# Performance work log

Measured on AMD Instinct MI355X. Metric: run time of the kernel, lower is better.

The kernel has to match this reference:

```python
import jax, jax.numpy as jnp
import numpy as np

N, E, D = 50000, 800000, 128
EPS = 1e-5  # PyG BatchNorm default eps


def setup_inputs() -> dict:
    key = jax.random.key(0)
    ks = jax.random.split(key, 12)
    s = 1.0 / np.sqrt(D)
    x = jax.random.normal(ks[0], (N, D), jnp.float32)
    edge_index = jax.random.randint(ks[1], (2, E), 0, N, dtype=jnp.int32)
    Wp = jax.random.normal(ks[2], (D, D), jnp.float32) * s
    bp = jax.random.normal(ks[3], (D,), jnp.float32) * 0.01
    # 4 SAGEConv layers, all 128->128, stacked: lin_l (neighbor, with bias) and lin_r (root)
    Wl = jax.random.normal(ks[4], (4, D, D), jnp.float32) * s
    bl = jax.random.normal(ks[5], (4, D), jnp.float32) * 0.01
    Wr = jax.random.normal(ks[6], (4, D, D), jnp.float32) * s
    # BatchNorm params/buffers (eval mode: running stats)
    bn_gamma = 1.0 + 0.1 * jax.random.normal(ks[7], (4, D), jnp.float32)
    bn_beta = 0.1 * jax.random.normal(ks[8], (4, D), jnp.float32)
    bn_mean = 0.1 * jax.random.normal(ks[9], (4, D), jnp.float32)
    bn_var = jax.random.uniform(ks[10], (4, D), jnp.float32, 0.5, 1.5)
    return {"x": x, "edge_index": edge_index, "Wp": Wp, "bp": bp, "Wl": Wl,
            "bl": bl, "Wr": Wr, "bn_gamma": bn_gamma, "bn_beta": bn_beta,
            "bn_mean": bn_mean, "bn_var": bn_var}


def _sage_conv(x, src, dst, inv_deg, Wl, bl, Wr):
    # mean-aggregate neighbor features: gather x[src], scatter-sum to dst, divide by degree
    agg = jax.ops.segment_sum(x[src], dst, num_segments=N) * inv_deg  # [N, D]
    # PyG SAGEConv: lin_l(aggr) + lin_r(x_root)
    return agg @ Wl + bl + x @ Wr


def _bn(h, gamma, beta, mean, var):
    return (h - mean) * (gamma * jax.lax.rsqrt(var + EPS)) + beta


def reference(x, edge_index, Wp, bp, Wl, bl, Wr, bn_gamma, bn_beta, bn_mean, bn_var):
    src, dst = edge_index[0], edge_index[1]
    deg = jax.ops.segment_sum(jnp.ones((E,), x.dtype), dst, num_segments=N)
    inv_deg = (1.0 / jnp.maximum(deg, 1.0))[:, None]  # [N, 1]
    x = jax.nn.relu(x @ Wp + bp)
    # eval mode: dropout is identity, BN uses running stats
    for i in range(3):
        h = _sage_conv(x, src, dst, inv_deg, Wl[i], bl[i], Wr[i])
        h = jax.nn.relu(_bn(h, bn_gamma[i], bn_beta[i], bn_mean[i], bn_var[i]))
        x = x + h
    x = _sage_conv(x, src, dst, inv_deg, Wl[3], bl[3], Wr[3])
    return jax.nn.relu(_bn(x, bn_gamma[3], bn_beta[3], bn_mean[3], bn_var[3]))
```

## Files before the change

kernel.cpp:

```cpp
#include <hip/hip_runtime.h>

#define DIM 128
#define BN_EPS 1e-5f
#define BCAP 8192
#define EPB 4096
#define EPT 16

typedef __bf16 bf16x8 __attribute__((ext_vector_type(8)));
typedef float f32x4 __attribute__((ext_vector_type(4)));
typedef float f32x2 __attribute__((ext_vector_type(2)));

__device__ __forceinline__ float bf_e0(unsigned int u) {
    return __builtin_bit_cast(float, u << 16);
}
__device__ __forceinline__ float bf_e1(unsigned int u) {
    return __builtin_bit_cast(float, u & 0xffff0000u);
}
__device__ __forceinline__ unsigned short f2b(float f) {
    __bf16 b = (__bf16)f;
    return __builtin_bit_cast(unsigned short, b);
}
__device__ __forceinline__ unsigned int pack2(float lo, float hi) {
    return (unsigned int)f2b(lo) | ((unsigned int)f2b(hi) << 16);
}

__global__ __launch_bounds__(256) void k_bin(const int* __restrict__ src,
                                             const int* __restrict__ dst,
                                             int* __restrict__ cursor,
                                             unsigned int* __restrict__ binned,
                                             int E, int NB) {
    __shared__ int hist[256];
    __shared__ int base[256];
    __shared__ int c2[256];
    const int tid = threadIdx.x;
    const int e0 = blockIdx.x * EPB;

    unsigned int u[EPT];
    int b[EPT];
    hist[tid] = 0;
    c2[tid] = 0;
    __syncthreads();
#pragma unroll
    for (int i = 0; i < EPT; ++i) {
        int e = e0 + i * 256 + tid;
        if (e < E) {
            int d = dst[e];
            b[i] = d >> 8;
            u[i] = ((unsigned int)(d & 255) << 17) | (unsigned int)src[e];
            atomicAdd(&hist[b[i]], 1);
        } else {
            b[i] = -1;
        }
    }
    __syncthreads();
    if (tid < NB && hist[tid] > 0) base[tid] = atomicAdd(&cursor[tid], hist[tid]);
    __syncthreads();
#pragma unroll
    for (int i = 0; i < EPT; ++i) {
        if (b[i] < 0) continue;
        int p = base[b[i]] + atomicAdd(&c2[b[i]], 1);
        if (p < BCAP) binned[(size_t)b[i] * BCAP + p] = u[i];
    }
}

__global__ __launch_bounds__(256) void k_bscan(const int* __restrict__ cursor,
                                               int* __restrict__ bbase,
                                               int* __restrict__ rowptr, int NB,
                                               int N, int E) {
    __shared__ int sh[256];
    int t = threadIdx.x;
    int v = (t < NB) ? min(cursor[t], BCAP) : 0;
    sh[t] = v;
    __syncthreads();
    for (int off = 1; off < 256; off <<= 1) {
        int a = (t >= off) ? sh[t - off] : 0;
        __syncthreads();
        sh[t] += a;
        __syncthreads();
    }
    if (t < NB) bbase[t] = sh[t] - v;
    if (t == 0) rowptr[N] = E;
}

__global__ __launch_bounds__(256) void k_csr(const int* __restrict__ cursor,
                                             const int* __restrict__ bbase,
                                             const unsigned int* __restrict__ binned,
                                             int* __restrict__ rowptr,
                                             float* __restrict__ inv_deg,
                                             int* __restrict__ col, int N) {
    __shared__ unsigned int stage[BCAP];
    __shared__ int deg[256];
    __shared__ int start[256];
    const int b = blockIdx.x;
    const int t = threadIdx.x;
    const int node0 = b << 8;
    const int cnt = min(cursor[b], BCAP);
    const int gbase = bbase[b];

    deg[t] = 0;
    __syncthreads();
    for (int e = t; e < cnt; e += 256) {
        unsigned int u = binned[(size_t)b * BCAP + e];
        stage[e] = u;
        atomicAdd(&deg[u >> 17], 1);
    }
    __syncthreads();
    int d = deg[t];
    start[t] = d;
    __syncthreads();
    for (int off = 1; off < 256; off <<= 1) {
        int a = (t >= off) ? start[t - off] : 0;
        __syncthreads();
        start[t] += a;
        __syncthreads();
    }
    int excl = start[t] - d;
    int node = node0 + t;
    if (node < N) {
        rowptr[node] = gbase + excl;
        inv_deg[node] = 1.0f / (float)(d > 1 ? d : 1);
    }
    __syncthreads();
    deg[t] = excl;
    __syncthreads();
    for (int e = t; e < cnt; e += 256) {
        unsigned int u = stage[e];
        int dl = u >> 17;
        int p = atomicAdd(&deg[dl], 1);
        col[gbase + p] = (int)(u & 0x1ffffu);
    }
}

__global__ void k_wtr(const float* __restrict__ Wp, const float* __restrict__ Wl,
                      const float* __restrict__ Wr, unsigned short* __restrict__ WTf) {
    int gid = blockIdx.x * blockDim.x + threadIdx.x;
    if (gid >= 9 * 2048) return;
    int m = gid >> 11;
    int r = gid & 2047;
    int lane = r & 63;
    int k = (r >> 6) & 3;
    int ct = r >> 8;
    int feat = ct * 16 + (lane & 15);
    int kb = k * 32 + (lane >> 4) * 8;
    const float* W = (m == 0) ? Wp : (m < 5) ? (Wl + (size_t)(m - 1) * DIM * DIM)
                                             : (Wr + (size_t)(m - 5) * DIM * DIM);
    unsigned short o[8];
#pragma unroll
    for (int e = 0; e < 8; ++e) o[e] = f2b(W[(size_t)(kb + e) * DIM + feat]);
    *(uint4*)(WTf + (size_t)gid * 8) = *(const uint4*)o;
}

__global__ void k_agg(const uint2* __restrict__ x8_2, const int* __restrict__ rowptr,
                      const int* __restrict__ col, const float* __restrict__ inv_deg,
                      uint4* __restrict__ aggb4, int n) {
    int node = (blockIdx.x * blockDim.x + threadIdx.x) >> 6;
    int lane = threadIdx.x & 63;
    if (node >= n) return;
    const int e4 = lane >> 4, c16 = lane & 15;
    const int lo = rowptr[node], hi = rowptr[node + 1];

    float a0 = 0.f, a1 = 0.f, a2 = 0.f, a3 = 0.f,
          a4 = 0.f, a5 = 0.f, a6 = 0.f, a7 = 0.f;

    int i0 = lo + e4;
    int s0 = (i0      < hi) ? col[i0]      : -1;
    int s1 = (i0 + 4  < hi) ? col[i0 + 4]  : -1;
    int s2 = (i0 + 8  < hi) ? col[i0 + 8]  : -1;
    int s3 = (i0 + 12 < hi) ? col[i0 + 12] : -1;

    for (int j = lo; j < hi; j += 16) {
        uint2 v0 = x8_2[(size_t)(s0 > 0 ? s0 : 0) * 16 + c16];
        uint2 v1 = x8_2[(size_t)(s1 > 0 ? s1 : 0) * 16 + c16];
        uint2 v2 = x8_2[(size_t)(s2 > 0 ? s2 : 0) * 16 + c16];
        uint2 v3 = x8_2[(size_t)(s3 > 0 ? s3 : 0) * 16 + c16];
        float m0 = s0 >= 0 ? 1.f : 0.f;
        float m1 = s1 >= 0 ? 1.f : 0.f;
        float m2 = s2 >= 0 ? 1.f : 0.f;
        float m3 = s3 >= 0 ? 1.f : 0.f;
        int nj = j + 16 + e4;
        s0 = (nj      < hi) ? col[nj]      : -1;
        s1 = (nj + 4  < hi) ? col[nj + 4]  : -1;
        s2 = (nj + 8  < hi) ? col[nj + 8]  : -1;
        s3 = (nj + 12 < hi) ? col[nj + 12] : -1;
#define ACC_(v, m)                                                            \
        {                                                                     \
            f32x2 f01 = __builtin_amdgcn_cvt_pk_f32_fp8(v.x, false);          \
            f32x2 f23 = __builtin_amdgcn_cvt_pk_f32_fp8(v.x, true);           \
            f32x2 f45 = __builtin_amdgcn_cvt_pk_f32_fp8(v.y, false);          \
            f32x2 f67 = __builtin_amdgcn_cvt_pk_f32_fp8(v.y, true);           \
            a0 = fmaf(f01.x, m, a0); a1 = fmaf(f01.y, m, a1);                 \
            a2 = fmaf(f23.x, m, a2); a3 = fmaf(f23.y, m, a3);                 \
            a4 = fmaf(f45.x, m, a4); a5 = fmaf(f45.y, m, a5);                 \
            a6 = fmaf(f67.x, m, a6); a7 = fmaf(f67.y, m, a7);                 \
        }
        ACC_(v0, m0) ACC_(v1, m1) ACC_(v2, m2) ACC_(v3, m3)
#undef ACC_
    }
#define RED_(a) a += __shfl_xor(a, 16); a += __shfl_xor(a, 32);
    RED_(a0) RED_(a1) RED_(a2) RED_(a3) RED_(a4) RED_(a5) RED_(a6) RED_(a7)
#undef RED_
    float sc = inv_deg[node];
    uint4 o;
    o.x = pack2(a0 * sc, a1 * sc);
    o.y = pack2(a2 * sc, a3 * sc);
    o.z = pack2(a4 * sc, a5 * sc);
    o.w = pack2(a6 * sc, a7 * sc);
    if (lane < 16) aggb4[(size_t)node * 16 + c16] = o;
}

template <int NSEG, bool A0F32>
__global__ __launch_bounds__(256) void k_gemm(
    const void* __restrict__ A0v, const unsigned short* __restrict__ A1,
    const unsigned short* __restrict__ Wf0, const unsigned short* __restrict__ Wf1,
    const float* __restrict__ bias,
    const float* __restrict__ gamma, const float* __restrict__ beta,
    const float* __restrict__ mean, const float* __restrict__ var,
    const unsigned short* __restrict__ residb,
    float* __restrict__ out32, unsigned short* __restrict__ outb,
    unsigned char* __restrict__ out8, int nrows) {
    __shared__ unsigned short wlds[16384];
    __shared__ float colp[2 * DIM];

    const int tid = threadIdx.x;
    const int lane = tid & 63;
    const int l15 = lane & 15;
    const int lhi = lane >> 4;
    const int wave = tid >> 6;
    const int node = blockIdx.x * 64 + wave * 16 + l15;
    const int arow = node < nrows ? node : nrows - 1;

    if (tid < DIM) {
        float sc, sh;
        if (gamma) {
            float s = gamma[tid] * rsqrtf(var[tid] + BN_EPS);
            sc = s;
            sh = (bias[tid] - mean[tid]) * s + beta[tid];
        } else {
            sc = 1.f;
            sh = bias[tid];
        }
        colp[tid * 2] = sc;
        colp[tid * 2 + 1] = sh;
    }

    f32x4 acc[8];
#pragma unroll
    for (int ct = 0; ct < 8; ++ct) acc[ct] = (f32x4){0.f, 0.f, 0.f, 0.f};

    {
        const uint4* g = (const uint4*)Wf0;
        uint4* l = (uint4*)wlds;
#pragma unroll
        for (int i = 0; i < 8; ++i) l[tid + i * 256] = g[tid + i * 256];
    }
    __syncthreads();

    {
        bf16x8 af[4];
        if (A0F32) {
            const float* a0 = (const float*)A0v + (size_t)arow * DIM + lhi * 8;
#pragma unroll
            for (int k = 0; k < 4; ++k) {
                float4 v0 = *(const float4*)(a0 + k * 32);
                float4 v1 = *(const float4*)(a0 + k * 32 + 4);
                bf16x8 f;
                f[0] = (__bf16)v0.x; f[1] = (__bf16)v0.y;
                f[2] = (__bf16)v0.z; f[3] = (__bf16)v0.w;
                f[4] = (__bf16)v1.x; f[5] = (__bf16)v1.y;
                f[6] = (__bf16)v1.z; f[7] = (__bf16)v1.w;
                af[k] = f;
            }
        } else {
            const unsigned short* a0 = (const unsigned short*)A0v + (size_t)arow * DIM + lhi * 8;
#pragma unroll
            for (int k = 0; k < 4; ++k) af[k] = *(const bf16x8*)(a0 + k * 32);
        }
#pragma unroll
        for (int k = 0; k < 4; ++k) {
            bf16x8 bw[8];
#pragma unroll
            for (int ct = 0; ct < 8; ++ct)
                bw[ct] = *(const bf16x8*)&wlds[((ct * 4 + k) * 64 + lane) * 8];
#pragma unroll
            for (int ct = 0; ct < 8; ++ct)
                acc[ct] = __builtin_amdgcn_mfma_f32_16x16x32_bf16(bw[ct], af[k],
                                                                  acc[ct], 0, 0, 0);
        }
    }

    if (NSEG == 2) {
        __syncthreads();
        {
            const uint4* g = (const uint4*)Wf1;
            uint4* l = (uint4*)wlds;
#pragma unroll
            for (int i = 0; i < 8; ++i) l[tid + i * 256] = g[tid + i * 256];
        }
        __syncthreads();
        bf16x8 af[4];
        const unsigned short* a1 = A1 + (size_t)arow * DIM + lhi * 8;
#pragma unroll
        for (int k = 0; k < 4; ++k) af[k] = *(const bf16x8*)(a1 + k * 32);
#pragma unroll
        for (int k = 0; k < 4; ++k) {
            bf16x8 bw[8];
#pragma unroll
            for (int ct = 0; ct < 8; ++ct)
                bw[ct] = *(const bf16x8*)&wlds[((ct * 4 + k) * 64 + lane) * 8];
#pragma unroll
            for (int ct = 0; ct < 8; ++ct)
                acc[ct] = __builtin_amdgcn_mfma_f32_16x16x32_bf16(bw[ct], af[k],
                                                                  acc[ct], 0, 0, 0);
        }
    } else {
        __syncthreads();
    }

    if (node < nrows) {
#pragma unroll
        for (int ct = 0; ct < 8; ++ct) {
            int c0 = ct * 16 + lhi * 4;
            float h[4];
#pragma unroll
            for (int j = 0; j < 4; ++j) {
                float2 p = *(const float2*)&colp[(c0 + j) * 2];
                h[j] = fmaxf(acc[ct][j] * p.x + p.y, 0.f);
            }
            size_t base = (size_t)node * DIM + c0;
            if (residb) {
                uint2 rv = *(const uint2*)(residb + base);
                h[0] += bf_e0(rv.x); h[1] += bf_e1(rv.x);
                h[2] += bf_e0(rv.y); h[3] += bf_e1(rv.y);
            }
            if (outb) {
                uint2 o;
                o.x = pack2(h[0], h[1]);
                o.y = pack2(h[2], h[3]);
                *(uint2*)(outb + base) = o;
            }
            if (out8) {
                int w = __builtin_amdgcn_cvt_pk_fp8_f32(h[0], h[1], 0, false);
                w = __builtin_amdgcn_cvt_pk_fp8_f32(h[2], h[3], w, true);
                *(unsigned int*)(out8 + base) = (unsigned int)w;
            }
            if (out32)
                *(float4*)(out32 + base) = make_float4(h[0], h[1], h[2], h[3]);
        }
    }
}

extern "C" void kernel_launch(void* const* d_in, const int* in_sizes, int n_in,
                              void* d_out, int out_size, void* d_ws, size_t ws_size,
                              hipStream_t stream) {
    const float* x_in = (const float*)d_in[0];
    const int* ei     = (const int*)d_in[1];
    const float* Wp   = (const float*)d_in[2];
    const float* bp   = (const float*)d_in[3];
    const float* Wl   = (const float*)d_in[4];
    const float* bl   = (const float*)d_in[5];
    const float* Wr   = (const float*)d_in[6];
    const float* g    = (const float*)d_in[7];
    const float* be   = (const float*)d_in[8];
    const float* mu   = (const float*)d_in[9];
    const float* va   = (const float*)d_in[10];

    const int N = in_sizes[0] / DIM;
    const int E = in_sizes[1] / 2;
    const int* src = ei;
    const int* dst = ei + E;
    const int NB = (N + 255) >> 8;

    char* p = (char*)d_ws;
    auto alloc = [&](size_t bytes) {
        char* r = p;
        p += (bytes + 255) & ~(size_t)255;
        return r;
    };
    float* inv_deg = (float*)alloc((size_t)N * 4);
    int* rowptr    = (int*)alloc((size_t)(N + 1) * 4);
    int* cursor    = (int*)alloc((size_t)NB * 4);
    int* bbase     = (int*)alloc((size_t)NB * 4);
    int* col       = (int*)alloc((size_t)E * 4);
    unsigned int* binned = (unsigned int*)alloc((size_t)NB * BCAP * 4);
    unsigned short* xb   = (unsigned short*)alloc((size_t)N * DIM * 2);
    unsigned char* x8    = (unsigned char*)alloc((size_t)N * DIM);
    unsigned short* aggb = (unsigned short*)alloc((size_t)N * DIM * 2);
    unsigned short* WTf  = (unsigned short*)alloc((size_t)9 * 16384 * 2);

    hipMemsetAsync(cursor, 0, (size_t)NB * 4, stream);
    k_bin<<<(E + EPB - 1) / EPB, 256, 0, stream>>>(src, dst, cursor, binned, E, NB);
    k_bscan<<<1, 256, 0, stream>>>(cursor, bbase, rowptr, NB, N, E);
    k_csr<<<NB, 256, 0, stream>>>(cursor, bbase, binned, rowptr, inv_deg, col, N);

    k_wtr<<<(9 * 2048 + 255) / 256, 256, 0, stream>>>(Wp, Wl, Wr, WTf);

    const int gblocks = (N + 63) / 64;

    k_gemm<1, true><<<gblocks, 256, 0, stream>>>(
        x_in, nullptr, WTf, nullptr, bp,
        nullptr, nullptr, nullptr, nullptr, nullptr,
        nullptr, xb, x8, N);

    float* out = (float*)d_out;
    for (int i = 0; i < 4; ++i) {
        k_agg<<<(N + 3) / 4, 256, 0, stream>>>((const uint2*)x8, rowptr, col,
                                               inv_deg, (uint4*)aggb, N);
        const unsigned short* WlF = WTf + (size_t)(1 + i) * 16384;
        const unsigned short* WrF = WTf + (size_t)(5 + i) * 16384;
        k_gemm<2, false><<<gblocks, 256, 0, stream>>>(
            aggb, xb, WlF, WrF, bl + i * DIM,
            g + i * DIM, be + i * DIM, mu + i * DIM, va + i * DIM,
            (i < 3) ? xb : nullptr,
            (i < 3) ? nullptr : out, (i < 3) ? xb : nullptr,
            (i < 3) ? x8 : nullptr, N);
    }
}
```

Measured before the change: 211.8 us.

## Fuse preprocessing kernels and stream GEMM weights directly into LDS with prefetch

Folds the weight transpose/convert into the edge-binning kernel and the bucket prefix scan into the CSR build kernel, removing two launches. Each CSR block redundantly recomputes the 256-entry scan. The GEMM kernel now issues activation loads before weight staging, uses global_load_lds to copy weights straight into LDS, and prefetches the second operand before the first MFMA segment. This trades extra registers and redundant scan work for fewer launches and better load/compute overlap.

```diff
diff --git a/kernel.cpp b/kernel.cpp
--- a/kernel.cpp
+++ b/kernel.cpp
@@ -24,10 +24,19 @@
     return (unsigned int)f2b(lo) | ((unsigned int)f2b(hi) << 16);
 }
 
+#define GLOAD_LDS16(gsrc, ldst)                                               \
+    __builtin_amdgcn_global_load_lds(                                         \
+        (const __attribute__((address_space(1))) void*)(gsrc),                \
+        (__attribute__((address_space(3))) void*)(ldst), 16, 0, 0)
+
 __global__ __launch_bounds__(256) void k_bin(const int* __restrict__ src,
                                              const int* __restrict__ dst,
                                              int* __restrict__ cursor,
                                              unsigned int* __restrict__ binned,
+                                             const float* __restrict__ Wp,
+                                             const float* __restrict__ Wl,
+                                             const float* __restrict__ Wr,
+                                             unsigned short* __restrict__ WTf,
                                              int E, int NB) {
     __shared__ int hist[256];
     __shared__ int base[256];
@@ -61,44 +70,52 @@
         int p = base[b[i]] + atomicAdd(&c2[b[i]], 1);
         if (p < BCAP) binned[(size_t)b[i] * BCAP + p] = u[i];
     }
-}
-
-__global__ __launch_bounds__(256) void k_bscan(const int* __restrict__ cursor,
-                                               int* __restrict__ bbase,
-                                               int* __restrict__ rowptr, int NB,
-                                               int N, int E) {
-    __shared__ int sh[256];
-    int t = threadIdx.x;
-    int v = (t < NB) ? min(cursor[t], BCAP) : 0;
-    sh[t] = v;
-    __syncthreads();
-    for (int off = 1; off < 256; off <<= 1) {
-        int a = (t >= off) ? sh[t - off] : 0;
-        __syncthreads();
-        sh[t] += a;
-        __syncthreads();
-    }
-    if (t < NB) bbase[t] = sh[t] - v;
-    if (t == 0) rowptr[N] = E;
+
+    int gid = blockIdx.x * 256 + tid;
+    if (gid < 9 * 2048) {
+        int m = gid >> 11;
+        int r = gid & 2047;
+        int lane = r & 63;
+        int k = (r >> 6) & 3;
+        int ct = r >> 8;
+        int feat = ct * 16 + (lane & 15);
+        int kb = k * 32 + (lane >> 4) * 8;
+        const float* W = (m == 0) ? Wp : (m < 5) ? (Wl + (size_t)(m - 1) * DIM * DIM)
+                                                 : (Wr + (size_t)(m - 5) * DIM * DIM);
+        unsigned short o[8];
+#pragma unroll
+        for (int e = 0; e < 8; ++e) o[e] = f2b(W[(size_t)(kb + e) * DIM + feat]);
+        *(uint4*)(WTf + (size_t)gid * 8) = *(const uint4*)o;
+    }
 }
 
 __global__ __launch_bounds__(256) void k_csr(const int* __restrict__ cursor,
-                                             const int* __restrict__ bbase,
                                              const unsigned int* __restrict__ binned,
                                              int* __restrict__ rowptr,
                                              float* __restrict__ inv_deg,
-                                             int* __restrict__ col, int N) {
+                                             int* __restrict__ col, int N, int NB) {
     __shared__ unsigned int stage[BCAP];
     __shared__ int deg[256];
     __shared__ int start[256];
+    __shared__ int sh[256];
     const int b = blockIdx.x;
     const int t = threadIdx.x;
     const int node0 = b << 8;
+
+    int v = (t < NB) ? min(cursor[t], BCAP) : 0;
+    sh[t] = v;
+    deg[t] = 0;
+    __syncthreads();
+    for (int off = 1; off < 256; off <<= 1) {
+        int a = (t >= off) ? sh[t - off] : 0;
+        __syncthreads();
+        sh[t] += a;
+        __syncthreads();
+    }
+    const int gbase = sh[b] - min(cursor[b], BCAP);
     const int cnt = min(cursor[b], BCAP);
-    const int gbase = bbase[b];
-
-    deg[t] = 0;
-    __syncthreads();
+    if (b == 0 && t == 255) rowptr[N] = sh[255];
+
     for (int e = t; e < cnt; e += 256) {
         unsigned int u = binned[(size_t)b * BCAP + e];
         stage[e] = u;
@@ -129,25 +146,6 @@
         int p = atomicAdd(&deg[dl], 1);
         col[gbase + p] = (int)(u & 0x1ffffu);
     }
-}
-
-__global__ void k_wtr(const float* __restrict__ Wp, const float* __restrict__ Wl,
-                      const float* __restrict__ Wr, unsigned short* __restrict__ WTf) {
-    int gid = blockIdx.x * blockDim.x + threadIdx.x;
-    if (gid >= 9 * 2048) return;
-    int m = gid >> 11;
-    int r = gid & 2047;
-    int lane = r & 63;
-    int k = (r >> 6) & 3;
-    int ct = r >> 8;
-    int feat = ct * 16 + (lane & 15);
-    int kb = k * 32 + (lane >> 4) * 8;
-    const float* W = (m == 0) ? Wp : (m < 5) ? (Wl + (size_t)(m - 1) * DIM * DIM)
-                                             : (Wr + (size_t)(m - 5) * DIM * DIM);
-    unsigned short o[8];
-#pragma unroll
-    for (int e = 0; e < 8; ++e) o[e] = f2b(W[(size_t)(kb + e) * DIM + feat]);
-    *(uint4*)(WTf + (size_t)gid * 8) = *(const uint4*)o;
 }
 
 __global__ void k_agg(const uint2* __restrict__ x8_2, const int* __restrict__ rowptr,
@@ -229,6 +227,33 @@
     const int node = blockIdx.x * 64 + wave * 16 + l15;
     const int arow = node < nrows ? node : nrows - 1;
 
+    bf16x8 af0[4];
+    if (A0F32) {
+        const float* a0 = (const float*)A0v + (size_t)arow * DIM + lhi * 8;
+#pragma unroll
+        for (int k = 0; k < 4; ++k) {
+            float4 v0 = *(const float4*)(a0 + k * 32);
+            float4 v1 = *(const float4*)(a0 + k * 32 + 4);
+            bf16x8 f;
+            f[0] = (__bf16)v0.x; f[1] = (__bf16)v0.y;
+            f[2] = (__bf16)v0.z; f[3] = (__bf16)v0.w;
+            f[4] = (__bf16)v1.x; f[5] = (__bf16)v1.y;
+            f[6] = (__bf16)v1.z; f[7] = (__bf16)v1.w;
+            af0[k] = f;
+        }
+    } else {
+        const unsigned short* a0 = (const unsigned short*)A0v + (size_t)arow * DIM + lhi * 8;
+#pragma unroll
+        for (int k = 0; k < 4; ++k) af0[k] = *(const bf16x8*)(a0 + k * 32);
+    }
+
+    {
+        const unsigned short* g = Wf0 + (size_t)wave * 4096 + lane * 8;
+#pragma unroll
+        for (int i = 0; i < 8; ++i)
+            GLOAD_LDS16(g + i * 512, &wlds[wave * 4096 + i * 512]);
+    }
+
     if (tid < DIM) {
         float sc, sh;
         if (gamma) {
@@ -247,34 +272,36 @@
 #pragma unroll
     for (int ct = 0; ct < 8; ++ct) acc[ct] = (f32x4){0.f, 0.f, 0.f, 0.f};
 
-    {
-        const uint4* g = (const uint4*)Wf0;
-        uint4* l = (uint4*)wlds;
-#pragma unroll
-        for (int i = 0; i < 8; ++i) l[tid + i * 256] = g[tid + i * 256];
-    }
-    __syncthreads();
-
-    {
-        bf16x8 af[4];
-        if (A0F32) {
-            const float* a0 = (const float*)A0v + (size_t)arow * DIM + lhi * 8;
-#pragma unroll
-            for (int k = 0; k < 4; ++k) {
-                float4 v0 = *(const float4*)(a0 + k * 32);
-                float4 v1 = *(const float4*)(a0 + k * 32 + 4);
-                bf16x8 f;
-                f[0] = (__bf16)v0.x; f[1] = (__bf16)v0.y;
-                f[2] = (__bf16)v0.z; f[3] = (__bf16)v0.w;
-                f[4] = (__bf16)v1.x; f[5] = (__bf16)v1.y;
-                f[6] = (__bf16)v1.z; f[7] = (__bf16)v1.w;
-                af[k] = f;
-            }
-        } else {
-            const unsigned short* a0 = (const unsigned short*)A0v + (size_t)arow * DIM + lhi * 8;
-#pragma unroll
-            for (int k = 0; k < 4; ++k) af[k] = *(const bf16x8*)(a0 + k * 32);
-        }
+    __syncthreads();
+
+    bf16x8 af1[4];
+    if (NSEG == 2) {
+        const unsigned short* a1 = A1 + (size_t)arow * DIM + lhi * 8;
+#pragma unroll
+        for (int k = 0; k < 4; ++k) af1[k] = *(const bf16x8*)(a1 + k * 32);
+    }
+
+#pragma unroll
+    for (int k = 0; k < 4; ++k) {
+        bf16x8 bw[8];
+#pragma unroll
+        for (int ct = 0; ct < 8; ++ct)
+            bw[ct] = *(const bf16x8*)&wlds[((ct * 4 + k) * 64 + lane) * 8];
+#pragma unroll
+        for (int ct = 0; ct < 8; ++ct)
+            acc[ct] = __builtin_amdgcn_mfma_f32_16x16x32_bf16(bw[ct], af0[k],
+                                                              acc[ct], 0, 0, 0);
+    }
+
+    if (NSEG == 2) {
+        __syncthreads();
+        {
+            const unsigned short* g = Wf1 + (size_t)wave * 4096 + lane * 8;
+#pragma unroll
+            for (int i = 0; i < 8; ++i)
+                GLOAD_LDS16(g + i * 512, &wlds[wave * 4096 + i * 512]);
+        }
+        __syncthreads();
 #pragma unroll
         for (int k = 0; k < 4; ++k) {
             bf16x8 bw[8];
@@ -283,37 +310,9 @@
                 bw[ct] = *(const bf16x8*)&wlds[((ct * 4 + k) * 64 + lane) * 8];
 #pragma unroll
             for (int ct = 0; ct < 8; ++ct)
-                acc[ct] = __builtin_amdgcn_mfma_f32_16x16x32_bf16(bw[ct], af[k],
+                acc[ct] = __builtin_amdgcn_mfma_f32_16x16x32_bf16(bw[ct], af1[k],
                                                                   acc[ct], 0, 0, 0);
         }
-    }
-
-    if (NSEG == 2) {
-        __syncthreads();
-        {
-            const uint4* g = (const uint4*)Wf1;
-            uint4* l = (uint4*)wlds;
-#pragma unroll
-            for (int i = 0; i < 8; ++i) l[tid + i * 256] = g[tid + i * 256];
-        }
-        __syncthreads();
-        bf16x8 af[4];
-        const unsigned short* a1 = A1 + (size_t)arow * DIM + lhi * 8;
-#pragma unroll
-        for (int k = 0; k < 4; ++k) af[k] = *(const bf16x8*)(a1 + k * 32);
-#pragma unroll
-        for (int k = 0; k < 4; ++k) {
-            bf16x8 bw[8];
-#pragma unroll
-            for (int ct = 0; ct < 8; ++ct)
-                bw[ct] = *(const bf16x8*)&wlds[((ct * 4 + k) * 64 + lane) * 8];
-#pragma unroll
-            for (int ct = 0; ct < 8; ++ct)
-                acc[ct] = __builtin_amdgcn_mfma_f32_16x16x32_bf16(bw[ct], af[k],
-                                                                  acc[ct], 0, 0, 0);
-        }
-    } else {
-        __syncthreads();
     }
 
     if (node < nrows) {
@@ -379,7 +378,6 @@
     float* inv_deg = (float*)alloc((size_t)N * 4);
     int* rowptr    = (int*)alloc((size_t)(N + 1) * 4);
     int* cursor    = (int*)alloc((size_t)NB * 4);
-    int* bbase     = (int*)alloc((size_t)NB * 4);
     int* col       = (int*)alloc((size_t)E * 4);
     unsigned int* binned = (unsigned int*)alloc((size_t)NB * BCAP * 4);
     unsigned short* xb   = (unsigned short*)alloc((size_t)N * DIM * 2);
@@ -388,11 +386,9 @@
     unsigned short* WTf  = (unsigned short*)alloc((size_t)9 * 16384 * 2);
 
     hipMemsetAsync(cursor, 0, (size_t)NB * 4, stream);
-    k_bin<<<(E + EPB - 1) / EPB, 256, 0, stream>>>(src, dst, cursor, binned, E, NB);
-    k_bscan<<<1, 256, 0, stream>>>(cursor, bbase, rowptr, NB, N, E);
-    k_csr<<<NB, 256, 0, stream>>>(cursor, bbase, binned, rowptr, inv_deg, col, N);
-
-    k_wtr<<<(9 * 2048 + 255) / 256, 256, 0, stream>>>(Wp, Wl, Wr, WTf);
+    k_bin<<<(E + EPB - 1) / EPB, 256, 0, stream>>>(src, dst, cursor, binned,
+                                                   Wp, Wl, Wr, WTf, E, NB);
+    k_csr<<<NB, 256, 0, stream>>>(cursor, binned, rowptr, inv_deg, col, N, NB);
 
     const int gblocks = (N + 63) / 64;
 
```

Measured after the change: 209.6 us. About the same (-1.0%).
